# Optimization experiments

Hardware: AMD Instinct MI355X
Metric: run time of the kernel (lower is better)

The kernel has to match this reference:

```python
import jax, jax.numpy as jnp
import numpy as np

D_MODEL = 1024
NUM_HEADS = 16
HEAD_DIM = D_MODEL // NUM_HEADS
FF_HIDDEN = 2 * D_MODEL
EPS = 1e-5


def _layernorm(x, g, b):
    mu = jnp.mean(x, axis=-1, keepdims=True)
    var = jnp.var(x, axis=-1, keepdims=True)
    return (x - mu) * jax.lax.rsqrt(var + EPS) * g + b


def setup_inputs() -> dict:
    key = jax.random.key(0)
    ks = jax.random.split(key, 12)
    s = lambda fan_in: 1.0 / np.sqrt(fan_in)
    return {
        "x": jax.random.normal(ks[0], (4, 2048, D_MODEL), dtype=jnp.float32),
        "qkv_w": jax.random.uniform(ks[1], (D_MODEL, 3 * D_MODEL), minval=-s(D_MODEL), maxval=s(D_MODEL)),
        "qkv_b": jax.random.uniform(ks[2], (3 * D_MODEL,), minval=-s(D_MODEL), maxval=s(D_MODEL)),
        "out_w": jax.random.uniform(ks[3], (D_MODEL, D_MODEL), minval=-s(D_MODEL), maxval=s(D_MODEL)),
        "out_b": jax.random.uniform(ks[4], (D_MODEL,), minval=-s(D_MODEL), maxval=s(D_MODEL)),
        "ff1_w": jax.random.uniform(ks[5], (D_MODEL, FF_HIDDEN), minval=-s(D_MODEL), maxval=s(D_MODEL)),
        "ff1_b": jax.random.uniform(ks[6], (FF_HIDDEN,), minval=-s(D_MODEL), maxval=s(D_MODEL)),
        "ff2_w": jax.random.uniform(ks[7], (FF_HIDDEN, D_MODEL), minval=-s(FF_HIDDEN), maxval=s(FF_HIDDEN)),
        "ff2_b": jax.random.uniform(ks[8], (D_MODEL,), minval=-s(FF_HIDDEN), maxval=s(FF_HIDDEN)),
        "ln1_g": jnp.ones((D_MODEL,), jnp.float32),
        "ln1_b": jnp.zeros((D_MODEL,), jnp.float32),
        "ln2_g": jnp.ones((D_MODEL,), jnp.float32),
        "ln2_b": jnp.zeros((D_MODEL,), jnp.float32),
    }


def reference(x, qkv_w, qkv_b, out_w, out_b, ff1_w, ff1_b, ff2_w, ff2_b, ln1_g, ln1_b, ln2_g, ln2_b):
    B, L, _ = x.shape
    scale = HEAD_DIM ** -0.5
    # pre-norm attention
    h = _layernorm(x, ln1_g, ln1_b)
    qkv = h @ qkv_w + qkv_b  # [B,L,3D]
    q, k, v = jnp.split(qkv, 3, axis=-1)
    reshape = lambda t: t.reshape(B, L, NUM_HEADS, HEAD_DIM).transpose(0, 2, 1, 3)  # [B,H,L,Dh]
    q, k, v = reshape(q), reshape(k), reshape(v)
    attn = jnp.einsum('bhqd,bhkd->bhqk', q, k) * scale  # [B,H,L,L]
    attn = jax.nn.softmax(attn, axis=-1)
    ctx = jnp.einsum('bhqk,bhkd->bhqd', attn, v)
    ctx = ctx.transpose(0, 2, 1, 3).reshape(B, L, D_MODEL)
    attended = ctx @ out_w + out_b
    x = x + attended
    # pre-norm FFN with exact GELU (torch default)
    h2 = _layernorm(x, ln2_g, ln2_b)
    ff = jax.nn.gelu(h2 @ ff1_w + ff1_b, approximate=False) @ ff2_w + ff2_b
    return x + ff
```

## Files before the change

### kernel.cpp

```cpp
#include <hip/hip_runtime.h>

#define AS1 __attribute__((address_space(1)))
#define AS3 __attribute__((address_space(3)))

typedef unsigned short u16;
typedef __bf16 bf16x8 __attribute__((ext_vector_type(8)));
typedef float floatx4 __attribute__((ext_vector_type(4)));
typedef float floatx16 __attribute__((ext_vector_type(16)));
typedef u16 u16x8 __attribute__((ext_vector_type(8)));
typedef u16 u16x4 __attribute__((ext_vector_type(4)));
typedef unsigned uintx4 __attribute__((ext_vector_type(4)));

__device__ __forceinline__ float bf2f(u16 u) { return __uint_as_float(((unsigned)u) << 16); }
__device__ __forceinline__ u16 f2bf(float f) {
    unsigned u = __float_as_uint(f);
    u += 0x7FFFu + ((u >> 16) & 1u);
    return (u16)(u >> 16);
}
__device__ __forceinline__ unsigned packbf2(float f0, float f1) {
    return __builtin_amdgcn_perm(__float_as_uint(f1), __float_as_uint(f0), 0x07060302u);
}
__device__ __forceinline__ float fexp2(float x) {
#if __has_builtin(__builtin_amdgcn_exp2f)
    return __builtin_amdgcn_exp2f(x);
#else
    float r;
    asm("v_exp_f32 %0, %1" : "=v"(r) : "v"(x));
    return r;
#endif
}
__device__ __forceinline__ void gl_lds16(const u16* g, u16* l) {
    __builtin_amdgcn_global_load_lds((const AS1 void*)g, (AS3 void*)l, 16, 0, 0);
}

__global__ __launch_bounds__(256) void transpose_all(const float* __restrict__ w0, u16* __restrict__ o0,
                                                     const float* __restrict__ w1, u16* __restrict__ o1,
                                                     const float* __restrict__ w2, u16* __restrict__ o2,
                                                     const float* __restrict__ w3, u16* __restrict__ o3) {
    __shared__ u16 t[32][33];
    int blk = blockIdx.x;
    const float* in;
    u16* out;
    int R, C, bx, by;
    if (blk < 3072) {
        in = w0; out = o0; R = 1024; C = 3072; bx = blk % 96; by = blk / 96;
    } else if (blk < 4096) {
        blk -= 3072; in = w1; out = o1; R = 1024; C = 1024; bx = blk % 32; by = blk / 32;
    } else if (blk < 6144) {
        blk -= 4096; in = w2; out = o2; R = 1024; C = 2048; bx = blk % 64; by = blk / 64;
    } else {
        blk -= 6144; in = w3; out = o3; R = 2048; C = 1024; bx = blk % 32; by = blk / 32;
    }
    const int c0 = bx * 32, r0 = by * 32;
    const int tx = threadIdx.x, ty = threadIdx.y;
#pragma unroll
    for (int i = 0; i < 4; i++)
        t[ty + i * 8][tx] = f2bf(in[(size_t)(r0 + ty + i * 8) * C + c0 + tx]);
    __syncthreads();
#pragma unroll
    for (int i = 0; i < 4; i++) out[(size_t)(c0 + ty + i * 8) * R + r0 + tx] = t[tx][ty + i * 8];
}

__global__ __launch_bounds__(256) void ln_k(const float* __restrict__ x, const float* __restrict__ g,
                                            const float* __restrict__ b, u16* __restrict__ out) {
    const int row = blockIdx.x, tid = threadIdx.x;
    const float4 xv = *(const float4*)(x + (size_t)row * 1024 + tid * 4);
    float f[4] = {xv.x, xv.y, xv.z, xv.w};
    float s1 = 0.f, s2 = 0.f;
#pragma unroll
    for (int e = 0; e < 4; e++) {
        s1 += f[e];
        s2 += f[e] * f[e];
    }
#pragma unroll
    for (int off = 32; off >= 1; off >>= 1) {
        s1 += __shfl_down(s1, off);
        s2 += __shfl_down(s2, off);
    }
    __shared__ float w1[4], w2[4];
    const int wave = tid >> 6, lane = tid & 63;
    if (lane == 0) { w1[wave] = s1; w2[wave] = s2; }
    __syncthreads();
    s1 = w1[0] + w1[1] + w1[2] + w1[3];
    s2 = w2[0] + w2[1] + w2[2] + w2[3];
    const float mu = s1 * (1.0f / 1024.0f);
    const float var = s2 * (1.0f / 1024.0f) - mu * mu;
    const float rs = rsqrtf(var + 1e-5f);
    const float4 gv = *(const float4*)(g + tid * 4);
    const float4 bv = *(const float4*)(b + tid * 4);
    const float gf[4] = {gv.x, gv.y, gv.z, gv.w}, bff[4] = {bv.x, bv.y, bv.z, bv.w};
    u16x4 o;
#pragma unroll
    for (int e = 0; e < 4; e++) o[e] = f2bf((f[e] - mu) * rs * gf[e] + bff[e]);
    *(u16x4*)(out + (size_t)row * 1024 + tid * 4) = o;
}

template <int GELU, int RESID, int F32OUT, int KSWZ>
__global__ __launch_bounds__(256, 4) void gemm_bt(const u16* __restrict__ A, const u16* __restrict__ Bt,
                                                  const float* __restrict__ bias,
                                                  const float* __restrict__ resid, void* __restrict__ Cv,
                                                  int M, int N, int K, int lda) {
    __shared__ u16 Al[2][128 * 32];
    __shared__ u16 Bl[2][128 * 32];
    const int tid = threadIdx.x;
    const int wave = tid >> 6, lane = tid & 63;
    const int g16 = lane >> 4, l16 = lane & 15;
    const int nwgx = gridDim.x;
    int id = blockIdx.y * nwgx + blockIdx.x;
    const int cpx = (nwgx * gridDim.y) >> 3;
    id = (id & 7) * cpx + (id >> 3);
    const int m0 = (id / nwgx) * 128, n0 = (id % nwgx) * 128;
    const int wm = (wave >> 1) * 64, wn = (wave & 1) * 64;
    const int csw = (l16 >> 1) & 3;

    floatx4 acc[4][4] = {};

    const int scs = ((lane & 3) ^ ((lane >> 3) & 3)) * 8;
    const u16* Ag = A + (size_t)(m0 + (lane >> 2)) * lda + scs;
    const u16* Bg = Bt + (size_t)(n0 + (lane >> 2)) * K + scs;

    auto stage = [&](int buf, int k0) {
#pragma unroll
        for (int i = 0; i < 2; i++) {
            const int ro = 16 * (wave * 2 + i);
            gl_lds16(Ag + (size_t)ro * lda + k0, &Al[buf][(wave * 2 + i) * 512]);
            gl_lds16(Bg + (size_t)ro * K + k0, &Bl[buf][(wave * 2 + i) * 512]);
        }
    };

    stage(0, 0);
    __syncthreads();
    int buf = 0;
    for (int k0 = 0; k0 < K; k0 += 32) {
        if (k0 + 32 < K) stage(buf ^ 1, k0 + 32);
        bf16x8 af[4], bfr[4];
#pragma unroll
        for (int i = 0; i < 4; i++)
            af[i] = *(const bf16x8*)&Al[buf][(wm + i * 16 + l16) * 32 + ((g16 ^ csw) << 3)];
#pragma unroll
        for (int j = 0; j < 4; j++)
            bfr[j] = *(const bf16x8*)&Bl[buf][(wn + j * 16 + l16) * 32 + ((g16 ^ csw) << 3)];
#pragma unroll
        for (int i = 0; i < 4; i++)
#pragma unroll
            for (int j = 0; j < 4; j++)
                acc[i][j] = __builtin_amdgcn_mfma_f32_16x16x32_bf16(af[i], bfr[j], acc[i][j], 0, 0, 0);
        __syncthreads();
        buf ^= 1;
    }

    float bv[4];
#pragma unroll
    for (int j = 0; j < 4; j++) bv[j] = bias[n0 + wn + j * 16 + l16];
#pragma unroll
    for (int i = 0; i < 4; i++) {
#pragma unroll
        for (int r = 0; r < 4; r++) {
            const int gm = m0 + wm + i * 16 + g16 * 4 + r;
            const size_t ro = (size_t)gm * N;
#pragma unroll
            for (int j = 0; j < 4; j++) {
                int gn = n0 + wn + j * 16 + l16;
                float v = acc[i][j][r] + bv[j];
                if (GELU) v = 0.5f * v * (1.0f + erff(v * 0.70710678118654752f));
                if (RESID) v += resid[ro + gn];
                if (KSWZ && ((gn >> 10) == 1)) gn ^= (gm & 7) << 3;
                if (F32OUT)
                    ((float*)Cv)[ro + gn] = v;
                else
                    ((u16*)Cv)[ro + gn] = f2bf(v);
            }
        }
    }
}

__global__ __launch_bounds__(256) void attn_prep(const u16* __restrict__ qkv, u16* __restrict__ Vsw) {
    __shared__ u16 Tl[64][72];
    const int bh = blockIdx.y, b = bh >> 4, h = bh & 15;
    const int kt = blockIdx.x * 64;
    const int t = threadIdx.x;
    const size_t qbase = (size_t)b * 2048 * 3072;
    const int r = t >> 2, cpi = (t & 3) * 2;

    const u16* vrow = qkv + qbase + (size_t)(kt + r) * 3072 + 2048 + h * 64;
    *(u16x8*)&Tl[r][cpi * 8] = *(const u16x8*)(vrow + cpi * 8);
    *(u16x8*)&Tl[r][(cpi + 1) * 8] = *(const u16x8*)(vrow + (cpi + 1) * 8);
    __syncthreads();
    {
        const int d = r;
        u16* dst = Vsw + ((size_t)bh * 64 + d) * 2048 + kt;
#pragma unroll
        for (int i = 0; i < 2; i++) {
            const int cp = cpi + i;
            const int c = cp ^ (d & 7);
            u16x8 tmp;
#pragma unroll
            for (int e = 0; e < 8; e++) tmp[e] = Tl[c * 8 + e][d];
            *(u16x8*)(dst + cp * 8) = tmp;
        }
    }
}

__global__ __launch_bounds__(256, 4) void attn_k(u16* __restrict__ qkv, const u16* __restrict__ Vsw) {
    __shared__ u16 Kl[2][64 * 64];
    __shared__ u16 Vt[2][64 * 64];
    const int tid = threadIdx.x;
    const int w = tid >> 6, lane = tid & 63;
    const int l31 = lane & 31, half = lane >> 5, swz = lane & 7;
    const int bh = blockIdx.y, b = bh >> 4, h = bh & 15;
    const int q0 = blockIdx.x * 128 + w * 32;
    const size_t qbase = (size_t)b * 2048 * 3072;
    const size_t vbase = (size_t)bh * 64 * 2048;

    bf16x8 bq[4];
    {
        const u16* qp = qkv + qbase + (size_t)(q0 + l31) * 3072 + h * 64;
        const float sc = 0.125f * 1.44269504088896340736f;
#pragma unroll
        for (int kd = 0; kd < 4; kd++) {
            const u16x8 raw = *(const u16x8*)(qp + kd * 16 + half * 8);
            u16 tmp[8];
#pragma unroll
            for (int e = 0; e < 8; e++) tmp[e] = f2bf(bf2f(raw[e]) * sc);
            bq[kd] = *(const bf16x8*)tmp;
        }
    }

    floatx16 accO[2] = {};
    float lsp[4] = {0.f, 0.f, 0.f, 0.f};

    auto stage = [&](int buf, int kt) {
#pragma unroll
        for (int i = 0; i < 2; i++) {
            const int rr = w * 16 + i * 8 + (lane >> 3);
            gl_lds16(qkv + qbase + (size_t)(kt + rr) * 3072 + 1024 + h * 64 + (lane & 7) * 8,
                     &Kl[buf][(w * 16 + i * 8) * 64]);
            gl_lds16(Vsw + vbase + (size_t)rr * 2048 + kt + (lane & 7) * 8,
                     &Vt[buf][(w * 16 + i * 8) * 64]);
        }
    };

    auto qk = [&](int bufi, floatx16* S) {
        floatx16 t[2] = {};
#pragma unroll
        for (int kb = 0; kb < 2; kb++)
#pragma unroll
            for (int kd = 0; kd < 4; kd++) {
                const bf16x8 ak =
                    *(const bf16x8*)&Kl[bufi][(kb * 32 + l31) * 64 + ((kd * 2 + half) ^ swz) * 8];
                t[kb] = __builtin_amdgcn_mfma_f32_32x32x16_bf16(ak, bq[kd], t[kb], 0, 0, 0);
            }
        S[0] = t[0];
        S[1] = t[1];
    };

    auto fused_sm_pv = [&](int bufi, const floatx16* S) {
#pragma unroll
        for (int kb = 0; kb < 2; kb++)
#pragma unroll
            for (int kp = 0; kp < 2; kp++) {
                float E[8];
#pragma unroll
                for (int j = 0; j < 8; j++) {
                    E[j] = fexp2(S[kb][8 * kp + j]);
                    lsp[j & 3] += E[j];
                }
                unsigned x0 = packbf2(E[0], E[1]);
                unsigned x1 = packbf2(E[2], E[3]);
                unsigned y0 = packbf2(E[4], E[5]);
                unsigned y1 = packbf2(E[6], E[7]);
                asm volatile("v_permlane32_swap_b32 %0, %1" : "+v"(x0), "+v"(y0));
                asm volatile("v_permlane32_swap_b32 %0, %1" : "+v"(x1), "+v"(y1));
                uintx4 f;
                f[0] = x0; f[1] = x1; f[2] = y0; f[3] = y1;
                const bf16x8 bp = __builtin_bit_cast(bf16x8, f);
                const int kd = kb * 2 + kp;
#pragma unroll
                for (int db = 0; db < 2; db++) {
                    const bf16x8 av =
                        *(const bf16x8*)&Vt[bufi][(db * 32 + l31) * 64 + ((kd * 2 + half) ^ swz) * 8];
                    accO[db] = __builtin_amdgcn_mfma_f32_32x32x16_bf16(av, bp, accO[db], 0, 0, 0);
                }
            }
    };

    stage(0, 0);
    __syncthreads();
    stage(1, 64);
    floatx16 accS[2];
    qk(0, accS);

    int buf = 0;
    for (int kt = 0; kt < 2048 - 64; kt += 64) {
        fused_sm_pv(buf, accS);
        __syncthreads();
        if (kt + 128 < 2048) stage(buf, kt + 128);
        __builtin_amdgcn_s_setprio(1);
        qk(buf ^ 1, accS);
        __builtin_amdgcn_s_setprio(0);
        buf ^= 1;
    }
    fused_sm_pv(buf, accS);

    float lsum = (lsp[0] + lsp[1]) + (lsp[2] + lsp[3]);
    lsum += __shfl_xor(lsum, 32);
    const float rinv = 1.0f / lsum;
    u16* cw = qkv + qbase + (size_t)(q0 + l31) * 3072 + 2048 + h * 64;
#pragma unroll
    for (int db = 0; db < 2; db++)
#pragma unroll
        for (int rg = 0; rg < 4; rg++) {
            const int d0 = db * 32 + 8 * rg + 4 * half;
            u16x4 o;
#pragma unroll
            for (int rr2 = 0; rr2 < 4; rr2++) o[rr2] = f2bf(accO[db][rg * 4 + rr2] * rinv);
            *(u16x4*)(cw + d0) = o;
        }
}

extern "C" void kernel_launch(void* const* d_in, const int* in_sizes, int n_in, void* d_out,
                              int out_size, void* d_ws, size_t ws_size, hipStream_t stream) {
    const float* x = (const float*)d_in[0];
    const float* qkv_w = (const float*)d_in[1];
    const float* qkv_b = (const float*)d_in[2];
    const float* out_w = (const float*)d_in[3];
    const float* out_b = (const float*)d_in[4];
    const float* ff1_w = (const float*)d_in[5];
    const float* ff1_b = (const float*)d_in[6];
    const float* ff2_w = (const float*)d_in[7];
    const float* ff2_b = (const float*)d_in[8];
    const float* ln1_g = (const float*)d_in[9];
    const float* ln1_b = (const float*)d_in[10];
    const float* ln2_g = (const float*)d_in[11];
    const float* ln2_b = (const float*)d_in[12];
    float* out = (float*)d_out;

    char* ws = (char*)d_ws;
    u16* qkvT = (u16*)(ws);
    u16* outT = (u16*)(ws + 6291456);
    u16* ff1T = (u16*)(ws + 8388608);
    u16* ff2T = (u16*)(ws + 12582912);
    u16* hbuf = (u16*)(ws + 16777216);
    u16* big  = (u16*)(ws + 33554432);

    transpose_all<<<8192, dim3(32, 8), 0, stream>>>(qkv_w, qkvT, out_w, outT, ff1_w, ff1T, ff2_w, ff2T);

    ln_k<<<8192, 256, 0, stream>>>(x, ln1_g, ln1_b, hbuf);
    gemm_bt<0, 0, 0, 1><<<dim3(24, 64), 256, 0, stream>>>(hbuf, qkvT, qkv_b, nullptr, big, 8192, 3072, 1024, 1024);
    attn_prep<<<dim3(32, 64), 256, 0, stream>>>(big, hbuf);
    attn_k<<<dim3(16, 64), 256, 0, stream>>>(big, hbuf);
    gemm_bt<0, 1, 1, 0><<<dim3(8, 64), 256, 0, stream>>>(big + 2048, outT, out_b, x, out, 8192, 1024, 1024, 3072);
    ln_k<<<8192, 256, 0, stream>>>(out, ln2_g, ln2_b, hbuf);
    gemm_bt<1, 0, 0, 0><<<dim3(16, 64), 256, 0, stream>>>(hbuf, ff1T, ff1_b, nullptr, big, 8192, 2048, 1024, 1024);
    gemm_bt<0, 1, 1, 0><<<dim3(8, 64), 256, 0, stream>>>(big, ff2T, ff2_b, out, out, 8192, 1024, 2048, 2048);
}
```

Measured before the change: 422.5 us.

## Triple-buffer K/V tiles and overlap next QK with current softmax-PV

The attention kernel moves from double to triple-buffered K/V shared-memory tiles. The main loop is fully unrolled into a rotation with two score register sets, so the QK MFMAs for the next tile are issued alongside the exp/PV work for the current one, and loads run two tiles ahead. The aim is to hide LDS and global load latency and keep the matrix units busy across phases. In exchange it uses more shared memory and registers, and lowers the occupancy bound from 4 to 3 blocks per CU.

```diff
diff --git a/kernel.cpp b/kernel.cpp
--- a/kernel.cpp
+++ b/kernel.cpp
@@ -201,9 +201,9 @@
     }
 }
 
-__global__ __launch_bounds__(256, 4) void attn_k(u16* __restrict__ qkv, const u16* __restrict__ Vsw) {
-    __shared__ u16 Kl[2][64 * 64];
-    __shared__ u16 Vt[2][64 * 64];
+__global__ __launch_bounds__(256, 3) void attn_k(u16* __restrict__ qkv, const u16* __restrict__ Vsw) {
+    __shared__ u16 Kl[3 * 64 * 64];
+    __shared__ u16 Vt[3 * 64 * 64];
     const int tid = threadIdx.x;
     const int w = tid >> 6, lane = tid & 63;
     const int l31 = lane & 31, half = lane >> 5, swz = lane & 7;
@@ -228,79 +228,85 @@
 
     floatx16 accO[2] = {};
     float lsp[4] = {0.f, 0.f, 0.f, 0.f};
+    floatx16 sA[2], sB[2];
 
     auto stage = [&](int buf, int kt) {
 #pragma unroll
         for (int i = 0; i < 2; i++) {
             const int rr = w * 16 + i * 8 + (lane >> 3);
             gl_lds16(qkv + qbase + (size_t)(kt + rr) * 3072 + 1024 + h * 64 + (lane & 7) * 8,
-                     &Kl[buf][(w * 16 + i * 8) * 64]);
+                     Kl + buf * 4096 + (w * 16 + i * 8) * 64);
             gl_lds16(Vsw + vbase + (size_t)rr * 2048 + kt + (lane & 7) * 8,
-                     &Vt[buf][(w * 16 + i * 8) * 64]);
+                     Vt + buf * 4096 + (w * 16 + i * 8) * 64);
         }
     };
 
-    auto qk = [&](int bufi, floatx16* S) {
-        floatx16 t[2] = {};
-#pragma unroll
-        for (int kb = 0; kb < 2; kb++)
-#pragma unroll
-            for (int kd = 0; kd < 4; kd++) {
-                const bf16x8 ak =
-                    *(const bf16x8*)&Kl[bufi][(kb * 32 + l31) * 64 + ((kd * 2 + half) ^ swz) * 8];
-                t[kb] = __builtin_amdgcn_mfma_f32_32x32x16_bf16(ak, bq[kd], t[kb], 0, 0, 0);
-            }
-        S[0] = t[0];
-        S[1] = t[1];
-    };
-
-    auto fused_sm_pv = [&](int bufi, const floatx16* S) {
-#pragma unroll
-        for (int kb = 0; kb < 2; kb++)
-#pragma unroll
-            for (int kp = 0; kp < 2; kp++) {
-                float E[8];
-#pragma unroll
-                for (int j = 0; j < 8; j++) {
-                    E[j] = fexp2(S[kb][8 * kp + j]);
-                    lsp[j & 3] += E[j];
-                }
-                unsigned x0 = packbf2(E[0], E[1]);
-                unsigned x1 = packbf2(E[2], E[3]);
-                unsigned y0 = packbf2(E[4], E[5]);
-                unsigned y1 = packbf2(E[6], E[7]);
-                asm volatile("v_permlane32_swap_b32 %0, %1" : "+v"(x0), "+v"(y0));
-                asm volatile("v_permlane32_swap_b32 %0, %1" : "+v"(x1), "+v"(y1));
-                uintx4 f;
-                f[0] = x0; f[1] = x1; f[2] = y0; f[3] = y1;
-                const bf16x8 bp = __builtin_bit_cast(bf16x8, f);
-                const int kd = kb * 2 + kp;
-#pragma unroll
-                for (int db = 0; db < 2; db++) {
-                    const bf16x8 av =
-                        *(const bf16x8*)&Vt[bufi][(db * 32 + l31) * 64 + ((kd * 2 + half) ^ swz) * 8];
-                    accO[db] = __builtin_amdgcn_mfma_f32_32x32x16_bf16(av, bp, accO[db], 0, 0, 0);
-                }
-            }
-    };
+#define QK_TO(Sdst, BUFI)                                                                        \
+    {                                                                                            \
+        floatx16 t0 = {}, t1 = {};                                                               \
+        _Pragma("unroll") for (int kd = 0; kd < 4; kd++) {                                       \
+            const bf16x8 ak0 =                                                                   \
+                *(const bf16x8*)&Kl[(BUFI)*4096 + (l31)*64 + ((kd * 2 + half) ^ swz) * 8];       \
+            t0 = __builtin_amdgcn_mfma_f32_32x32x16_bf16(ak0, bq[kd], t0, 0, 0, 0);              \
+            const bf16x8 ak1 =                                                                   \
+                *(const bf16x8*)&Kl[(BUFI)*4096 + (32 + l31) * 64 + ((kd * 2 + half) ^ swz) * 8];\
+            t1 = __builtin_amdgcn_mfma_f32_32x32x16_bf16(ak1, bq[kd], t1, 0, 0, 0);              \
+        }                                                                                        \
+        Sdst[0] = t0;                                                                            \
+        Sdst[1] = t1;                                                                            \
+    }
+
+#define SMPV(Ssrc, BUFI)                                                                         \
+    {                                                                                            \
+        _Pragma("unroll") for (int kb = 0; kb < 2; kb++) {                                       \
+            _Pragma("unroll") for (int kp = 0; kp < 2; kp++) {                                   \
+                float E[8];                                                                      \
+                _Pragma("unroll") for (int j = 0; j < 8; j++) {                                  \
+                    E[j] = fexp2(Ssrc[kb][8 * kp + j]);                                          \
+                    lsp[j & 3] += E[j];                                                          \
+                }                                                                                \
+                unsigned x0 = packbf2(E[0], E[1]);                                               \
+                unsigned x1 = packbf2(E[2], E[3]);                                               \
+                unsigned y0 = packbf2(E[4], E[5]);                                               \
+                unsigned y1 = packbf2(E[6], E[7]);                                               \
+                asm volatile("v_permlane32_swap_b32 %0, %1" : "+v"(x0), "+v"(y0));               \
+                asm volatile("v_permlane32_swap_b32 %0, %1" : "+v"(x1), "+v"(y1));               \
+                uintx4 f;                                                                        \
+                f[0] = x0; f[1] = x1; f[2] = y0; f[3] = y1;                                      \
+                const bf16x8 bp = __builtin_bit_cast(bf16x8, f);                                 \
+                const int kd = kb * 2 + kp;                                                      \
+                _Pragma("unroll") for (int db = 0; db < 2; db++) {                               \
+                    const bf16x8 av = *(const bf16x8*)&Vt[(BUFI)*4096 + (db * 32 + l31) * 64 +   \
+                                                          ((kd * 2 + half) ^ swz) * 8];          \
+                    accO[db] = __builtin_amdgcn_mfma_f32_32x32x16_bf16(av, bp, accO[db], 0, 0, 0);\
+                }                                                                                \
+            }                                                                                    \
+        }                                                                                        \
+    }
 
     stage(0, 0);
-    __syncthreads();
     stage(1, 64);
-    floatx16 accS[2];
-    qk(0, accS);
-
-    int buf = 0;
-    for (int kt = 0; kt < 2048 - 64; kt += 64) {
-        fused_sm_pv(buf, accS);
-        __syncthreads();
-        if (kt + 128 < 2048) stage(buf, kt + 128);
-        __builtin_amdgcn_s_setprio(1);
-        qk(buf ^ 1, accS);
-        __builtin_amdgcn_s_setprio(0);
-        buf ^= 1;
-    }
-    fused_sm_pv(buf, accS);
+    __syncthreads();
+    stage(2, 128);
+    QK_TO(sA, 0)
+
+    for (int i = 0; i < 4; i++) {
+        const int k6 = i * 6 * 64;
+        QK_TO(sB, 1) SMPV(sA, 0) __syncthreads(); stage(0, k6 + 3 * 64);
+        QK_TO(sA, 2) SMPV(sB, 1) __syncthreads(); stage(1, k6 + 4 * 64);
+        QK_TO(sB, 0) SMPV(sA, 2) __syncthreads(); stage(2, k6 + 5 * 64);
+        QK_TO(sA, 1) SMPV(sB, 0) __syncthreads(); stage(0, k6 + 6 * 64);
+        QK_TO(sB, 2) SMPV(sA, 1) __syncthreads(); stage(1, k6 + 7 * 64);
+        QK_TO(sA, 0) SMPV(sB, 2) __syncthreads(); stage(2, k6 + 8 * 64);
+    }
+    QK_TO(sB, 1) SMPV(sA, 0) __syncthreads(); stage(0, 27 * 64);
+    QK_TO(sA, 2) SMPV(sB, 1) __syncthreads(); stage(1, 28 * 64);
+    QK_TO(sB, 0) SMPV(sA, 2) __syncthreads(); stage(2, 29 * 64);
+    QK_TO(sA, 1) SMPV(sB, 0) __syncthreads(); stage(0, 30 * 64);
+    QK_TO(sB, 2) SMPV(sA, 1) __syncthreads(); stage(1, 31 * 64);
+    QK_TO(sA, 0) SMPV(sB, 2) __syncthreads();
+    QK_TO(sB, 1) SMPV(sA, 0) __syncthreads();
+    SMPV(sB, 1)
 
     float lsum = (lsp[0] + lsp[1]) + (lsp[2] + lsp[3]);
     lsum += __shfl_xor(lsum, 32);
@@ -316,6 +322,8 @@
             for (int rr2 = 0; rr2 < 4; rr2++) o[rr2] = f2bf(accO[db][rg * 4 + rr2] * rinv);
             *(u16x4*)(cw + d0) = o;
         }
+#undef QK_TO
+#undef SMPV
 }
 
 extern "C" void kernel_launch(void* const* d_in, const int* in_sizes, int n_in, void* d_out,
```

Result: slower. 532.4 us (+26.0%).
